# Optimization experiments

Hardware: AMD Instinct MI355X
Metric: run time of the kernel (lower is better)

Reference implementation:

```python
import jax, jax.numpy as jnp
import numpy as np

B, S, D = 2, 2048, 1024
QH, KVH, DH = 16, 4, 64
TOP_K = 128
ROPE_BASE = 10000.0


def _rope(x):
    # x: [B, H, S, DH]; standard LLaMA-style rotate-half RoPE, no freq scaling
    half = DH // 2
    inv_freq = 1.0 / (ROPE_BASE ** (jnp.arange(half, dtype=jnp.float32) / half))
    ang = jnp.arange(S, dtype=jnp.float32)[:, None] * inv_freq[None, :]  # [S, half]
    cos, sin = jnp.cos(ang), jnp.sin(ang)
    x1, x2 = x[..., :half], x[..., half:]
    return jnp.concatenate([x1 * cos - x2 * sin, x2 * cos + x1 * sin], axis=-1)


def setup_inputs() -> dict:
    key = jax.random.key(0)
    ks = jax.random.split(key, 5)
    return {
        "x": jax.random.normal(ks[0], (B, S, D), dtype=jnp.float32),
        "Wq": jax.random.normal(ks[1], (QH * DH, D), dtype=jnp.float32) * 0.02,
        "Wk": jax.random.normal(ks[2], (KVH * DH, D), dtype=jnp.float32) * 0.02,
        "Wv": jax.random.normal(ks[3], (KVH * DH, D), dtype=jnp.float32) * 0.02,
        "Wo": jax.random.normal(ks[4], (D, QH * DH), dtype=jnp.float32) * 0.02,
    }


def reference(x, Wq, Wk, Wv, Wo):
    # projections (Linear, no bias): y = x @ W.T
    q = (x @ Wq.T).reshape(B, S, QH, DH).transpose(0, 2, 1, 3)   # [B,QH,S,DH]
    k = (x @ Wk.T).reshape(B, S, KVH, DH).transpose(0, 2, 1, 3)  # [B,KVH,S,DH]
    v = (x @ Wv.T).reshape(B, S, KVH, DH).transpose(0, 2, 1, 3)
    q = _rope(q)
    k = _rope(k)
    # repeat_kv: GQA expand kv heads to q heads
    rep = QH // KVH
    k = jnp.repeat(k, rep, axis=1)
    v = jnp.repeat(v, rep, axis=1)
    scores = jnp.einsum("bhqd,bhkd->bhqk", q, k) / np.sqrt(DH)  # [B,QH,S,S]
    causal = jnp.triu(jnp.ones((S, S), dtype=bool), k=1)
    scores = jnp.where(causal, -jnp.inf, scores)
    # top-k masking before softmax: keep entries >= per-row k-th largest score
    top_vals = jax.lax.top_k(scores, TOP_K)[0]        # [B,QH,S,TOP_K]
    thr = top_vals[..., -1:]
    scores = jnp.where(scores < thr, -jnp.inf, scores)
    w = jax.nn.softmax(scores, axis=-1)
    out = jnp.einsum("bhqk,bhkd->bhqd", w, v)         # [B,QH,S,DH]
    out = out.transpose(0, 2, 1, 3).reshape(B, S, QH * DH)
    return out @ Wo.T
```

## Files before the change

### kernel.cpp

```cpp
#include <hip/hip_runtime.h>
#include <hip/hip_bf16.h>
#include <hip/hip_fp16.h>
#include <math.h>

constexpr int cB   = 2;
constexpr int cS   = 2048;
constexpr int cD   = 1024;
constexpr int cQH  = 16;
constexpr int cKVH = 4;
constexpr int cDH  = 64;
constexpr int cTOPK = 128;
constexpr int cM   = cB * cS;
constexpr int cNB  = cS / 64;
constexpr int cLSZ = 384;

constexpr int cTI  = 8;
constexpr int cSTR = 130;

constexpr int cNQ  = cQH * cDH;
constexpr int cNK  = cKVH * cDH;
constexpr int cNQKV = cNQ + 2 * cNK;

typedef __attribute__((ext_vector_type(8))) short short8;
typedef __attribute__((ext_vector_type(4))) float floatx4;
typedef _Float16 half8 __attribute__((ext_vector_type(8)));

__device__ inline ushort f2bf(float f) {
    unsigned u = __float_as_uint(f);
    return (ushort)((u + 0x7FFFu + ((u >> 16) & 1u)) >> 16);
}

constexpr int cE0 = cM * cD;
constexpr int cE1 = cE0 + cNQ * cD;
constexpr int cE2 = cE1 + cNK * cD;
constexpr int cE3 = cE2 + cNK * cD;
constexpr int cE4 = cE3 + cD * cQH * cDH;

__global__ void cast_all_bf16(const float* __restrict__ x,
                              const float* __restrict__ wq,
                              const float* __restrict__ wk,
                              const float* __restrict__ wv,
                              const float* __restrict__ wo,
                              ushort* __restrict__ dst) {
    const int i4 = (blockIdx.x * blockDim.x + threadIdx.x) * 4;
    if (i4 >= cE4) return;
    const float* s;
    int off;
    if (i4 < cE0)      { s = x;  off = i4; }
    else if (i4 < cE1) { s = wq; off = i4 - cE0; }
    else if (i4 < cE2) { s = wk; off = i4 - cE1; }
    else if (i4 < cE3) { s = wv; off = i4 - cE2; }
    else               { s = wo; off = i4 - cE3; }
    const float4 v = *(const float4*)(s + off);
    ushort4 r;
    r.x = f2bf(v.x); r.y = f2bf(v.y); r.z = f2bf(v.z); r.w = f2bf(v.w);
    *(ushort4*)(dst + i4) = r;
}

__global__ __launch_bounds__(256) void gemm_bf16_bt(
        const ushort* __restrict__ A, const ushort* __restrict__ W,
        float* __restrict__ C, int M, int N, int K) {
    __shared__ short As[4][128][8];
    __shared__ short Bs[4][128][8];

    const int tid  = threadIdx.x;
    const int lane = tid & 63;
    const int w    = tid >> 6;
    const int wm   = (w & 1) * 64;
    const int wn   = (w >> 1) * 64;
    const int m0   = blockIdx.y * 128;
    const int n0   = blockIdx.x * 128;

    const int quad = lane >> 4;
    const int l16  = lane & 15;

    floatx4 acc[4][4];
    #pragma unroll
    for (int mi = 0; mi < 4; ++mi)
        #pragma unroll
        for (int ni = 0; ni < 4; ++ni)
            acc[mi][ni] = (floatx4){0.f, 0.f, 0.f, 0.f};

    const int sr = tid >> 1;
    const int sh = (tid & 1) * 2;

    for (int k0 = 0; k0 < K; k0 += 32) {
        const ushort* sa = A + (size_t)(m0 + sr) * K + k0 + sh * 8;
        const short8 a0 = *(const short8*)sa;
        const short8 a1 = *(const short8*)(sa + 8);
        const ushort* sw = W + (size_t)(n0 + sr) * K + k0 + sh * 8;
        const short8 b0 = *(const short8*)sw;
        const short8 b1 = *(const short8*)(sw + 8);
        *(short8*)&As[sh][sr][0]     = a0;
        *(short8*)&As[sh + 1][sr][0] = a1;
        *(short8*)&Bs[sh][sr][0]     = b0;
        *(short8*)&Bs[sh + 1][sr][0] = b1;
        __syncthreads();

        short8 af[4], bf[4];
        #pragma unroll
        for (int mi = 0; mi < 4; ++mi)
            af[mi] = *(const short8*)&As[quad][wm + mi * 16 + l16][0];
        #pragma unroll
        for (int ni = 0; ni < 4; ++ni)
            bf[ni] = *(const short8*)&Bs[quad][wn + ni * 16 + l16][0];
        #pragma unroll
        for (int mi = 0; mi < 4; ++mi)
            #pragma unroll
            for (int ni = 0; ni < 4; ++ni)
                acc[mi][ni] = __builtin_amdgcn_mfma_f32_16x16x32_bf16(
                    af[mi], bf[ni], acc[mi][ni], 0, 0, 0);
        __syncthreads();
    }

    #pragma unroll
    for (int mi = 0; mi < 4; ++mi)
        #pragma unroll
        for (int ni = 0; ni < 4; ++ni)
            #pragma unroll
            for (int r = 0; r < 4; ++r) {
                const int row = m0 + wm + mi * 16 + quad * 4 + r;
                const int col = n0 + wn + ni * 16 + l16;
                C[(size_t)row * N + col] = acc[mi][ni][r];
            }
}

__global__ void rope_cast_f16(const float* __restrict__ src,
                              ushort* __restrict__ dst, int H, int total,
                              float scale, int srcStride) {
    int idx = blockIdx.x * blockDim.x + threadIdx.x;
    if (idx >= total) return;
    const int d   = idx & 31;
    const int h   = (idx >> 5) % H;
    const int row = idx / (32 * H);
    const int s   = row % cS;
    const float inv_freq = powf(10000.0f, -(float)d / 32.0f);
    const float ang = (float)s * inv_freq;
    const float c  = cosf(ang);
    const float si = sinf(ang);
    const float* p = src + (size_t)row * srcStride + (size_t)h * cDH;
    const float x1 = p[d];
    const float x2 = p[d + 32];
    const float r1 = (x1 * c - x2 * si) * scale;
    const float r2 = (x2 * c + x1 * si) * scale;
    ushort* o = dst + (size_t)row * H * cDH + (size_t)h * cDH;
    o[d]      = __builtin_bit_cast(ushort, (_Float16)r1);
    o[d + 32] = __builtin_bit_cast(ushort, (_Float16)r2);
}

__global__ void cast_f32_f16_strided(const float* __restrict__ src,
                                     ushort* __restrict__ dst,
                                     int total, int cols, int srcStride) {
    const int i4 = (blockIdx.x * blockDim.x + threadIdx.x) * 4;
    if (i4 >= total) return;
    const int row = i4 / cols;
    const int col = i4 - row * cols;
    const float4 v = *(const float4*)(src + (size_t)row * srcStride + col);
    ushort4 r;
    r.x = __builtin_bit_cast(ushort, (_Float16)v.x);
    r.y = __builtin_bit_cast(ushort, (_Float16)v.y);
    r.z = __builtin_bit_cast(ushort, (_Float16)v.z);
    r.w = __builtin_bit_cast(ushort, (_Float16)v.w);
    *(ushort4*)(dst + i4) = r;
}

__device__ inline unsigned fmap(float f) {
    unsigned u = __float_as_uint(f);
    return (u & 0x80000000u) ? ~u : (u | 0x80000000u);
}
__device__ inline float funmap(unsigned u) {
    unsigned v = (u & 0x80000000u) ? (u & 0x7FFFFFFFu) : ~u;
    return __uint_as_float(v);
}

__global__ __launch_bounds__(512) void attn_tile_kernel(
        const ushort* __restrict__ qf, const ushort* __restrict__ kf,
        const ushort* __restrict__ vf, ushort* __restrict__ out) {
    extern __shared__ char smem[];
    unsigned* stg = (unsigned*)smem;
    unsigned* klA = (unsigned*)smem;
    int*      jlA = (int*)(klA + cTI * cLSZ);

    const int lane = threadIdx.x & 63;
    const int wv   = __builtin_amdgcn_readfirstlane(threadIdx.x >> 6);

    const int x  = blockIdx.x;
    const int it = (cS / cTI - 1) - (x >> 5);
    const int bh = x & 31;
    const int h  = bh & 15;
    const int b  = bh >> 4;
    const int kvh = h >> 2;
    const int i0  = it * cTI;

    const size_t bS = (size_t)b * cS;
    const int l16   = lane & 15;
    const int quad  = lane >> 4;
    const int jperm = ((lane & 3) << 4) + (lane >> 2);
    const int i     = i0 + wv;

    const ushort* qp = qf + ((bS + i0 + (l16 & 7)) * cQH + h) * cDH + quad * 8;
    const half8 a0h = __builtin_bit_cast(half8, *(const uint4*)qp);
    const half8 a1h = __builtin_bit_cast(half8, *(const uint4*)(qp + 32));

    unsigned key[cNB];
    #pragma unroll
    for (int jb = 0; jb < cNB; ++jb) key[jb] = 0u;

    const int nk16   = ((i0 + cTI - 1) >> 4) + 1;
    const int nchunk = (nk16 + 7) >> 3;

    #pragma unroll
    for (int c = 0; c < 16; ++c) {
        if (c >= nchunk) break;
        const int  kb16  = (c << 3) + wv;
        if (kb16 < nk16) {
            const ushort* kp = kf + ((bS + (kb16 << 4) + l16) * cKVH + kvh) * cDH + quad * 8;
            const uint4 b0 = *(const uint4*)kp;
            const uint4 b1 = *(const uint4*)(kp + 32);
            floatx4 acc = (floatx4){0.f, 0.f, 0.f, 0.f};
            acc = __builtin_amdgcn_mfma_f32_16x16x32_f16(
                a0h, __builtin_bit_cast(half8, b0), acc, 0, 0, 0);
            acc = __builtin_amdgcn_mfma_f32_16x16x32_f16(
                a1h, __builtin_bit_cast(half8, b1), acc, 0, 0, 0);
            if (quad < 2) {
                const int jg = (kb16 << 4) + l16;
                unsigned* sp = stg + (c & 1) * (cTI * cSTR) + (wv << 4) + l16;
                #pragma unroll
                for (int r2 = 0; r2 < 4; ++r2) {
                    const int qrow = quad * 4 + r2;
                    sp[qrow * cSTR] = (jg <= i0 + qrow) ? fmap(acc[r2]) : 0u;
                }
            }
        }
        __syncthreads();
        {
            const unsigned* rp = stg + (c & 1) * (cTI * cSTR) + wv * cSTR;
            #pragma unroll
            for (int jj = 0; jj < 2; ++jj) {
                const int j = (c << 7) + (jj << 6) + jperm;
                const unsigned kr = rp[(jj << 6) + jperm];
                key[(c << 1) + jj] = (j <= i) ? kr : 0u;
            }
        }
    }
    __syncthreads();

    const int nb = (i >> 6) + 1;
    unsigned* kl = klA + wv * cLSZ;
    int*      jl = jlA + wv * cLSZ;
    const int vbase0 = (int)(((unsigned)bS * cKVH + kvh) * cDH);

    unsigned um = 0u, un = 0xFFFFFFFFu;
    #pragma unroll
    for (int jb = 0; jb < cNB; ++jb) {
        if (jb >= nb) break;
        const unsigned kk = key[jb];
        um = max(um, kk);
        un = min(un, kk ? kk : 0xFFFFFFFFu);
    }
    #pragma unroll
    for (int off = 32; off >= 1; off >>= 1) {
        um = max(um, (unsigned)__shfl_xor((int)um, off));
        un = min(un, (unsigned)__shfl_xor((int)un, off));
    }
    const float mrow = funmap(um);

    unsigned ustar;
    if (i < cTOPK) {
        ustar = un;
    } else {
        unsigned lo = un, hi = um;
        while (lo < hi) {
            const unsigned d   = hi - lo;
            const unsigned mid = lo + (d >> 1) + (d & 1u);
            int cnt2 = 0;
            #pragma unroll
            for (int jb = 0; jb < cNB; ++jb) {
                if (jb >= nb) break;
                cnt2 += __popcll(__ballot(key[jb] >= mid));
            }
            if (cnt2 == cTOPK) {
                unsigned mn = 0xFFFFFFFFu;
                #pragma unroll
                for (int jb = 0; jb < cNB; ++jb) {
                    if (jb >= nb) break;
                    const unsigned kk = key[jb];
                    mn = min(mn, (kk >= mid) ? kk : 0xFFFFFFFFu);
                }
                #pragma unroll
                for (int off = 32; off >= 1; off >>= 1)
                    mn = min(mn, (unsigned)__shfl_xor((int)mn, off));
                lo = mn;
                break;
            }
            if (cnt2 > cTOPK) lo = mid; else hi = mid - 1u;
        }
        ustar = lo;
    }

    const unsigned long long mlt = (1ull << lane) - 1ull;
    int base = 0;
    #pragma unroll
    for (int jb = 0; jb < cNB; ++jb) {
        if (jb >= nb) break;
        const int j = (jb << 6) + jperm;
        const bool keep = (j <= i) && (key[jb] >= ustar);
        const unsigned long long mk = __ballot(keep);
        const int pos = base + __popcll(mk & mlt);
        if (keep && pos < cLSZ) {
            kl[pos] = key[jb];
            jl[pos] = vbase0 + j * (cKVH * cDH);
        }
        base += __popcll(mk);
    }
    const int cnt = min(base, cLSZ);

    float zp = 0.f;
    for (int t = lane; t < cnt; t += 64) {
        const float s  = funmap(kl[t]);
        const float wt = __expf(s - mrow);
        ((float*)kl)[t] = wt;
        zp += wt;
    }
    #pragma unroll
    for (int off = 32; off >= 1; off >>= 1) zp += __shfl_xor(zp, off);
    const float invZ = 1.0f / zp;

    float ac0 = 0.f, ac1 = 0.f, ac2 = 0.f, ac3 = 0.f;
    float ac4 = 0.f, ac5 = 0.f, ac6 = 0.f, ac7 = 0.f;
    int t = 0;
    #pragma unroll 2
    for (; t + 7 < cnt; t += 8) {
        const float wt0 = ((float*)kl)[t];
        const float wt1 = ((float*)kl)[t + 1];
        const float wt2 = ((float*)kl)[t + 2];
        const float wt3 = ((float*)kl)[t + 3];
        const float wt4 = ((float*)kl)[t + 4];
        const float wt5 = ((float*)kl)[t + 5];
        const float wt6 = ((float*)kl)[t + 6];
        const float wt7 = ((float*)kl)[t + 7];
        const int vo0 = jl[t];
        const int vo1 = jl[t + 1];
        const int vo2 = jl[t + 2];
        const int vo3 = jl[t + 3];
        const int vo4 = jl[t + 4];
        const int vo5 = jl[t + 5];
        const int vo6 = jl[t + 6];
        const int vo7 = jl[t + 7];
        ac0 += wt0 * (float)__builtin_bit_cast(_Float16, vf[vo0 + lane]);
        ac1 += wt1 * (float)__builtin_bit_cast(_Float16, vf[vo1 + lane]);
        ac2 += wt2 * (float)__builtin_bit_cast(_Float16, vf[vo2 + lane]);
        ac3 += wt3 * (float)__builtin_bit_cast(_Float16, vf[vo3 + lane]);
        ac4 += wt4 * (float)__builtin_bit_cast(_Float16, vf[vo4 + lane]);
        ac5 += wt5 * (float)__builtin_bit_cast(_Float16, vf[vo5 + lane]);
        ac6 += wt6 * (float)__builtin_bit_cast(_Float16, vf[vo6 + lane]);
        ac7 += wt7 * (float)__builtin_bit_cast(_Float16, vf[vo7 + lane]);
    }
    for (; t < cnt; ++t) {
        const float wt = ((float*)kl)[t];
        const int   vo = jl[t];
        ac0 += wt * (float)__builtin_bit_cast(_Float16, vf[vo + lane]);
    }
    const float acc = ((ac0 + ac1) + (ac2 + ac3)) + ((ac4 + ac5) + (ac6 + ac7));
    out[((bS + i) * cQH + h) * cDH + lane] = f2bf(acc * invZ);
}

extern "C" void kernel_launch(void* const* d_in, const int* in_sizes, int n_in,
                              void* d_out, int out_size, void* d_ws, size_t ws_size,
                              hipStream_t stream) {
    const float* x  = (const float*)d_in[0];
    const float* Wq = (const float*)d_in[1];
    const float* Wk = (const float*)d_in[2];
    const float* Wv = (const float*)d_in[3];
    const float* Wo = (const float*)d_in[4];
    float* out = (float*)d_out;

    float*  qkvb = (float*)d_ws;
    ushort* xh   = (ushort*)(qkvb + (size_t)cM * cNQKV);
    ushort* Wqh  = xh  + (size_t)cM * cD;
    ushort* Wkh  = Wqh + (size_t)cNQ * cD;
    ushort* Wvh  = Wkh + (size_t)cNK * cD;
    ushort* Woh  = Wvh + (size_t)cNK * cD;
    ushort* abh  = Woh + (size_t)cD * cQH * cDH;
    ushort* qff  = abh + (size_t)cM * cQH * cDH;
    ushort* kff  = qff + (size_t)cM * cQH * cDH;
    ushort* vff  = kff + (size_t)cM * cKVH * cDH;

    dim3 blk(256);

    cast_all_bf16<<<(cE4 / 4 + 255) / 256, blk, 0, stream>>>(
        x, Wq, Wk, Wv, Wo, xh);

    gemm_bf16_bt<<<dim3(cNQKV / 128, cM / 128), blk, 0, stream>>>(
        xh, Wqh, qkvb, cM, cNQKV, cD);

    {
        const int totq = cM * cQH * 32;
        const int totk = cM * cKVH * 32;
        rope_cast_f16<<<(totq + 255) / 256, blk, 0, stream>>>(
            qkvb, qff, cQH, totq, 0.125f, cNQKV);
        rope_cast_f16<<<(totk + 255) / 256, blk, 0, stream>>>(
            qkvb + cNQ, kff, cKVH, totk, 1.0f, cNQKV);
        const int nv = cM * cNK;
        cast_f32_f16_strided<<<(nv / 4 + 255) / 256, blk, 0, stream>>>(
            qkvb + cNQ + cNK, vff, nv, cNK, cNQKV);
    }

    constexpr size_t aSMEM = (size_t)cTI * cLSZ * 8;
    static_assert(2 * cTI * cSTR * 4 <= (int)aSMEM, "staging must fit");
    attn_tile_kernel<<<dim3(32 * (cS / cTI)), dim3(512), aSMEM, stream>>>(
        qff, kff, vff, abh);

    gemm_bf16_bt<<<dim3(cD / 128, cM / 128), blk, 0, stream>>>(abh, Woh, out, cM, cD, cD);
}
```

Measured before the change: 531.8 us.

## Compute top-k P·V with dense MFMA over scattered probabilities and transposed V

The QKV GEMM epilogue now writes V directly as a transposed fp16 buffer, which removes the separate V cast kernel. In the attention kernel, each warp scatters its kept softmax weights into a dense fp16 row of length S in shared memory. All 8 warps then split the key range and run 16x16x32 f16 MFMAs against transposed V, and the partial results are reduced through shared memory. This replaces sparse gathered scalar FMAs with dense tensor-core work, but it processes the whole causal prefix and so does more total FLOPs. It also adds a zero-fill pass over the shared-memory rows and extra synchronisation.

```diff
diff --git a/kernel.cpp b/kernel.cpp
--- a/kernel.cpp
+++ b/kernel.cpp
@@ -16,10 +16,18 @@
 
 constexpr int cTI  = 8;
 constexpr int cSTR = 130;
+constexpr int cPST = 2056;
 
 constexpr int cNQ  = cQH * cDH;
 constexpr int cNK  = cKVH * cDH;
 constexpr int cNQKV = cNQ + 2 * cNK;
+constexpr int cVC0 = cNQ + cNK;
+
+constexpr int cPBY = cTI * cPST * 2;
+constexpr int cKLB = cPBY;
+constexpr int cJSB = cKLB + cTI * cLSZ * 4;
+constexpr int cZB  = cJSB + cTI * cLSZ * 2;
+constexpr int cSMEMA = cZB + 32;
 
 typedef __attribute__((ext_vector_type(8))) short short8;
 typedef __attribute__((ext_vector_type(4))) float floatx4;
@@ -123,6 +131,88 @@
                 const int col = n0 + wn + ni * 16 + l16;
                 C[(size_t)row * N + col] = acc[mi][ni][r];
             }
+}
+
+__global__ __launch_bounds__(256) void gemm_qkv_bf16(
+        const ushort* __restrict__ A, const ushort* __restrict__ W,
+        float* __restrict__ C, ushort* __restrict__ vt, int M, int N, int K) {
+    __shared__ short As[4][128][8];
+    __shared__ short Bs[4][128][8];
+
+    const int tid  = threadIdx.x;
+    const int lane = tid & 63;
+    const int w    = tid >> 6;
+    const int wm   = (w & 1) * 64;
+    const int wn   = (w >> 1) * 64;
+    const int m0   = blockIdx.y * 128;
+    const int n0   = blockIdx.x * 128;
+
+    const int quad = lane >> 4;
+    const int l16  = lane & 15;
+
+    floatx4 acc[4][4];
+    #pragma unroll
+    for (int mi = 0; mi < 4; ++mi)
+        #pragma unroll
+        for (int ni = 0; ni < 4; ++ni)
+            acc[mi][ni] = (floatx4){0.f, 0.f, 0.f, 0.f};
+
+    const int sr = tid >> 1;
+    const int sh = (tid & 1) * 2;
+
+    for (int k0 = 0; k0 < K; k0 += 32) {
+        const ushort* sa = A + (size_t)(m0 + sr) * K + k0 + sh * 8;
+        const short8 a0 = *(const short8*)sa;
+        const short8 a1 = *(const short8*)(sa + 8);
+        const ushort* sw = W + (size_t)(n0 + sr) * K + k0 + sh * 8;
+        const short8 b0 = *(const short8*)sw;
+        const short8 b1 = *(const short8*)(sw + 8);
+        *(short8*)&As[sh][sr][0]     = a0;
+        *(short8*)&As[sh + 1][sr][0] = a1;
+        *(short8*)&Bs[sh][sr][0]     = b0;
+        *(short8*)&Bs[sh + 1][sr][0] = b1;
+        __syncthreads();
+
+        short8 af[4], bf[4];
+        #pragma unroll
+        for (int mi = 0; mi < 4; ++mi)
+            af[mi] = *(const short8*)&As[quad][wm + mi * 16 + l16][0];
+        #pragma unroll
+        for (int ni = 0; ni < 4; ++ni)
+            bf[ni] = *(const short8*)&Bs[quad][wn + ni * 16 + l16][0];
+        #pragma unroll
+        for (int mi = 0; mi < 4; ++mi)
+            #pragma unroll
+            for (int ni = 0; ni < 4; ++ni)
+                acc[mi][ni] = __builtin_amdgcn_mfma_f32_16x16x32_bf16(
+                    af[mi], bf[ni], acc[mi][ni], 0, 0, 0);
+        __syncthreads();
+    }
+
+    #pragma unroll
+    for (int mi = 0; mi < 4; ++mi)
+        #pragma unroll
+        for (int ni = 0; ni < 4; ++ni) {
+            const int col  = n0 + wn + ni * 16 + l16;
+            const int rowb = m0 + wm + mi * 16 + quad * 4;
+            if (col < cVC0) {
+                #pragma unroll
+                for (int r = 0; r < 4; ++r)
+                    C[(size_t)(rowb + r) * N + col] = acc[mi][ni][r];
+            } else {
+                const int vcol = col - cVC0;
+                const int kvh  = vcol >> 6;
+                const int d    = vcol & 63;
+                const int bb   = rowb >> 11;
+                const int jj   = rowb & (cS - 1);
+                ushort4 pk;
+                pk.x = __builtin_bit_cast(ushort, (_Float16)acc[mi][ni][0]);
+                pk.y = __builtin_bit_cast(ushort, (_Float16)acc[mi][ni][1]);
+                pk.z = __builtin_bit_cast(ushort, (_Float16)acc[mi][ni][2]);
+                pk.w = __builtin_bit_cast(ushort, (_Float16)acc[mi][ni][3]);
+                *(ushort4*)(vt + (((size_t)(bb * cKVH + kvh) * cDH + d) << 11) + jj) = pk;
+            }
+        }
 }
 
 __global__ void rope_cast_f16(const float* __restrict__ src,
@@ -148,22 +238,6 @@
     o[d + 32] = __builtin_bit_cast(ushort, (_Float16)r2);
 }
 
-__global__ void cast_f32_f16_strided(const float* __restrict__ src,
-                                     ushort* __restrict__ dst,
-                                     int total, int cols, int srcStride) {
-    const int i4 = (blockIdx.x * blockDim.x + threadIdx.x) * 4;
-    if (i4 >= total) return;
-    const int row = i4 / cols;
-    const int col = i4 - row * cols;
-    const float4 v = *(const float4*)(src + (size_t)row * srcStride + col);
-    ushort4 r;
-    r.x = __builtin_bit_cast(ushort, (_Float16)v.x);
-    r.y = __builtin_bit_cast(ushort, (_Float16)v.y);
-    r.z = __builtin_bit_cast(ushort, (_Float16)v.z);
-    r.w = __builtin_bit_cast(ushort, (_Float16)v.w);
-    *(ushort4*)(dst + i4) = r;
-}
-
 __device__ inline unsigned fmap(float f) {
     unsigned u = __float_as_uint(f);
     return (u & 0x80000000u) ? ~u : (u | 0x80000000u);
@@ -175,11 +249,14 @@
 
 __global__ __launch_bounds__(512) void attn_tile_kernel(
         const ushort* __restrict__ qf, const ushort* __restrict__ kf,
-        const ushort* __restrict__ vf, ushort* __restrict__ out) {
+        const ushort* __restrict__ vt, ushort* __restrict__ out) {
     extern __shared__ char smem[];
+    ushort*   P   = (ushort*)smem;
     unsigned* stg = (unsigned*)smem;
-    unsigned* klA = (unsigned*)smem;
-    int*      jlA = (int*)(klA + cTI * cLSZ);
+    unsigned* klA = (unsigned*)(smem + cKLB);
+    ushort*   jsA = (ushort*)(smem + cJSB);
+    float*    par = (float*)(smem + cKLB);
+    float*    Zs  = (float*)(smem + cZB);
 
     const int lane = threadIdx.x & 63;
     const int wv   = __builtin_amdgcn_readfirstlane(threadIdx.x >> 6);
@@ -245,10 +322,17 @@
     }
     __syncthreads();
 
+    {
+        uint4 z4 = (uint4){0u, 0u, 0u, 0u};
+        uint4* P4 = (uint4*)smem;
+        #pragma unroll 2
+        for (int u = threadIdx.x; u < cPBY / 16; u += 512) P4[u] = z4;
+    }
+    __syncthreads();
+
     const int nb = (i >> 6) + 1;
     unsigned* kl = klA + wv * cLSZ;
-    int*      jl = jlA + wv * cLSZ;
-    const int vbase0 = (int)(((unsigned)bS * cKVH + kvh) * cDH);
+    ushort*   js = jsA + wv * cLSZ;
 
     unsigned um = 0u, un = 0xFFFFFFFFu;
     #pragma unroll
@@ -309,60 +393,60 @@
         const int pos = base + __popcll(mk & mlt);
         if (keep && pos < cLSZ) {
             kl[pos] = key[jb];
-            jl[pos] = vbase0 + j * (cKVH * cDH);
+            js[pos] = (ushort)j;
         }
         base += __popcll(mk);
     }
     const int cnt = min(base, cLSZ);
 
     float zp = 0.f;
+    ushort* Pw = P + wv * cPST;
     for (int t = lane; t < cnt; t += 64) {
         const float s  = funmap(kl[t]);
         const float wt = __expf(s - mrow);
-        ((float*)kl)[t] = wt;
         zp += wt;
+        Pw[js[t]] = __builtin_bit_cast(ushort, (_Float16)wt);
     }
     #pragma unroll
     for (int off = 32; off >= 1; off >>= 1) zp += __shfl_xor(zp, off);
-    const float invZ = 1.0f / zp;
-
-    float ac0 = 0.f, ac1 = 0.f, ac2 = 0.f, ac3 = 0.f;
-    float ac4 = 0.f, ac5 = 0.f, ac6 = 0.f, ac7 = 0.f;
-    int t = 0;
-    #pragma unroll 2
-    for (; t + 7 < cnt; t += 8) {
-        const float wt0 = ((float*)kl)[t];
-        const float wt1 = ((float*)kl)[t + 1];
-        const float wt2 = ((float*)kl)[t + 2];
-        const float wt3 = ((float*)kl)[t + 3];
-        const float wt4 = ((float*)kl)[t + 4];
-        const float wt5 = ((float*)kl)[t + 5];
-        const float wt6 = ((float*)kl)[t + 6];
-        const float wt7 = ((float*)kl)[t + 7];
-        const int vo0 = jl[t];
-        const int vo1 = jl[t + 1];
-        const int vo2 = jl[t + 2];
-        const int vo3 = jl[t + 3];
-        const int vo4 = jl[t + 4];
-        const int vo5 = jl[t + 5];
-        const int vo6 = jl[t + 6];
-        const int vo7 = jl[t + 7];
-        ac0 += wt0 * (float)__builtin_bit_cast(_Float16, vf[vo0 + lane]);
-        ac1 += wt1 * (float)__builtin_bit_cast(_Float16, vf[vo1 + lane]);
-        ac2 += wt2 * (float)__builtin_bit_cast(_Float16, vf[vo2 + lane]);
-        ac3 += wt3 * (float)__builtin_bit_cast(_Float16, vf[vo3 + lane]);
-        ac4 += wt4 * (float)__builtin_bit_cast(_Float16, vf[vo4 + lane]);
-        ac5 += wt5 * (float)__builtin_bit_cast(_Float16, vf[vo5 + lane]);
-        ac6 += wt6 * (float)__builtin_bit_cast(_Float16, vf[vo6 + lane]);
-        ac7 += wt7 * (float)__builtin_bit_cast(_Float16, vf[vo7 + lane]);
-    }
-    for (; t < cnt; ++t) {
-        const float wt = ((float*)kl)[t];
-        const int   vo = jl[t];
-        ac0 += wt * (float)__builtin_bit_cast(_Float16, vf[vo + lane]);
-    }
-    const float acc = ((ac0 + ac1) + (ac2 + ac3)) + ((ac4 + ac5) + (ac6 + ac7));
-    out[((bS + i) * cQH + h) * cDH + lane] = f2bf(acc * invZ);
+    if (lane == 0) Zs[wv] = zp;
+    __syncthreads();
+
+    const int nsl = ((i0 + cTI - 1) >> 5) + 1;
+    floatx4 pacc[4];
+    #pragma unroll
+    for (int db = 0; db < 4; ++db) pacc[db] = (floatx4){0.f, 0.f, 0.f, 0.f};
+
+    const ushort* vtb = vt + (((size_t)(b * cKVH + kvh)) << 17);
+    const int prow = (l16 & 7) * cPST;
+    for (int s = wv; s < nsl; s += 8) {
+        const half8 ap = __builtin_bit_cast(half8,
+            *(const uint4*)(P + prow + s * 32 + quad * 8));
+        #pragma unroll
+        for (int db = 0; db < 4; ++db) {
+            const half8 bp = __builtin_bit_cast(half8,
+                *(const uint4*)(vtb + (((size_t)(db * 16 + l16)) << 11) + s * 32 + quad * 8));
+            pacc[db] = __builtin_amdgcn_mfma_f32_16x16x32_f16(
+                ap, bp, pacc[db], 0, 0, 0);
+        }
+    }
+
+    if (quad < 2) {
+        #pragma unroll
+        for (int db = 0; db < 4; ++db)
+            #pragma unroll
+            for (int r = 0; r < 4; ++r)
+                par[wv * 512 + (quad * 4 + r) * 64 + db * 16 + l16] = pacc[db][r];
+    }
+    __syncthreads();
+
+    {
+        float a = 0.f;
+        #pragma unroll
+        for (int w8 = 0; w8 < 8; ++w8) a += par[w8 * 512 + wv * 64 + lane];
+        const float invZ = 1.0f / Zs[wv];
+        out[((bS + i) * cQH + h) * cDH + lane] = f2bf(a * invZ);
+    }
 }
 
 extern "C" void kernel_launch(void* const* d_in, const int* in_sizes, int n_in,
@@ -384,15 +468,15 @@
     ushort* abh  = Woh + (size_t)cD * cQH * cDH;
     ushort* qff  = abh + (size_t)cM * cQH * cDH;
     ushort* kff  = qff + (size_t)cM * cQH * cDH;
-    ushort* vff  = kff + (size_t)cM * cKVH * cDH;
+    ushort* vt   = kff + (size_t)cM * cKVH * cDH;
 
     dim3 blk(256);
 
     cast_all_bf16<<<(cE4 / 4 + 255) / 256, blk, 0, stream>>>(
         x, Wq, Wk, Wv, Wo, xh);
 
-    gemm_bf16_bt<<<dim3(cNQKV / 128, cM / 128), blk, 0, stream>>>(
-        xh, Wqh, qkvb, cM, cNQKV, cD);
+    gemm_qkv_bf16<<<dim3(cNQKV / 128, cM / 128), blk, 0, stream>>>(
+        xh, Wqh, qkvb, vt, cM, cNQKV, cD);
 
     {
         const int totq = cM * cQH * 32;
@@ -401,15 +485,12 @@
             qkvb, qff, cQH, totq, 0.125f, cNQKV);
         rope_cast_f16<<<(totk + 255) / 256, blk, 0, stream>>>(
             qkvb + cNQ, kff, cKVH, totk, 1.0f, cNQKV);
-        const int nv = cM * cNK;
-        cast_f32_f16_strided<<<(nv / 4 + 255) / 256, blk, 0, stream>>>(
-            qkvb + cNQ + cNK, vff, nv, cNK, cNQKV);
-    }
-
-    constexpr size_t aSMEM = (size_t)cTI * cLSZ * 8;
-    static_assert(2 * cTI * cSTR * 4 <= (int)aSMEM, "staging must fit");
-    attn_tile_kernel<<<dim3(32 * (cS / cTI)), dim3(512), aSMEM, stream>>>(
-        qff, kff, vff, abh);
+    }
+
+    static_assert(2 * cTI * cSTR * 4 <= cPBY, "staging must fit in P region");
+    static_assert(cKLB + 8 * 512 * 4 <= cZB, "partials must fit in kl/jsl");
+    attn_tile_kernel<<<dim3(32 * (cS / cTI)), dim3(512), cSMEMA, stream>>>(
+        qff, kff, vt, abh);
 
     gemm_bf16_bt<<<dim3(cD / 128, cM / 128), blk, 0, stream>>>(abh, Woh, out, cM, cD, cD);
 }
```

New measurement: 541.1 us. Within noise of the previous version (+1.8%).

## Use direct global-to-LDS loads with swizzle in GEMM; prefetch K in scoring

Applied to the files above, without the earlier changes.

The bf16 GEMM now loads tiles straight into LDS with global_load_lds using an XOR-swizzled layout, and reads MFMA fragments through matching swizzled offsets. This skips the register round trip and is meant to reduce LDS bank conflicts. The top-k scoring loop software-prefetches the next K block into registers. It also moves the fmap key transform and causal masking from the staging write to the staging read. The swizzle index math is intricate and a wrong mapping would silently corrupt results.

```diff
diff --git a/kernel.cpp b/kernel.cpp
--- a/kernel.cpp
+++ b/kernel.cpp
@@ -28,6 +28,12 @@
 __device__ inline ushort f2bf(float f) {
     unsigned u = __float_as_uint(f);
     return (ushort)((u + 0x7FFFu + ((u >> 16) & 1u)) >> 16);
+}
+
+__device__ __forceinline__ void glds16(const ushort* g, ushort* l) {
+    __builtin_amdgcn_global_load_lds(
+        (const __attribute__((address_space(1))) unsigned int*)g,
+        (__attribute__((address_space(3))) unsigned int*)l, 16, 0, 0);
 }
 
 constexpr int cE0 = cM * cD;
@@ -60,8 +66,8 @@
 __global__ __launch_bounds__(256) void gemm_bf16_bt(
         const ushort* __restrict__ A, const ushort* __restrict__ W,
         float* __restrict__ C, int M, int N, int K) {
-    __shared__ short As[4][128][8];
-    __shared__ short Bs[4][128][8];
+    __shared__ ushort AsL[128 * 32];
+    __shared__ ushort BsL[128 * 32];
 
     const int tid  = threadIdx.x;
     const int lane = tid & 63;
@@ -70,9 +76,45 @@
     const int wn   = (w >> 1) * 64;
     const int m0   = blockIdx.y * 128;
     const int n0   = blockIdx.x * 128;
-
     const int quad = lane >> 4;
     const int l16  = lane & 15;
+
+    int r0, q0, r1, q1;
+    {
+        const int g5 = (w * 128 + lane) & 31;
+        const int b4 = (g5 >> 4) & 1, b3 = (g5 >> 3) & 1, b2 = (g5 >> 2) & 1;
+        const int b1 = (g5 >> 1) & 1, b0 = g5 & 1;
+        r0 = ((w * 128 + lane) >> 5) * 8 + ((b4 << 2) | (b3 << 1) | (b2 ^ b4));
+        q0 = ((b1 ^ b3) << 1) | (b0 ^ b2 ^ b4);
+    }
+    {
+        const int gI = w * 128 + 64 + lane;
+        const int g5 = gI & 31;
+        const int b4 = (g5 >> 4) & 1, b3 = (g5 >> 3) & 1, b2 = (g5 >> 2) & 1;
+        const int b1 = (g5 >> 1) & 1, b0 = g5 & 1;
+        r1 = (gI >> 5) * 8 + ((b4 << 2) | (b3 << 1) | (b2 ^ b4));
+        q1 = ((b1 ^ b3) << 1) | (b0 ^ b2 ^ b4);
+    }
+    const size_t aOff0 = (size_t)(m0 + r0) * K + q0 * 8;
+    const size_t aOff1 = (size_t)(m0 + r1) * K + q1 * 8;
+    const size_t bOff0 = (size_t)(n0 + r0) * K + q0 * 8;
+    const size_t bOff1 = (size_t)(n0 + r1) * K + q1 * 8;
+    ushort* ldsA0 = AsL + w * 1024;
+    ushort* ldsA1 = AsL + w * 1024 + 512;
+    ushort* ldsB0 = BsL + w * 1024;
+    ushort* ldsB1 = BsL + w * 1024 + 512;
+
+    int eA[4], eB[4];
+    #pragma unroll
+    for (int mi = 0; mi < 4; ++mi) {
+        const int rr = wm + mi * 16 + l16;
+        eA[mi] = (((rr >> 3) * 32) + ((4 * (rr & 7) + quad) ^ (rr & 7))) * 8;
+    }
+    #pragma unroll
+    for (int ni = 0; ni < 4; ++ni) {
+        const int rn = wn + ni * 16 + l16;
+        eB[ni] = (((rn >> 3) * 32) + ((4 * (rn & 7) + quad) ^ (rn & 7))) * 8;
+    }
 
     floatx4 acc[4][4];
     #pragma unroll
@@ -81,29 +123,20 @@
         for (int ni = 0; ni < 4; ++ni)
             acc[mi][ni] = (floatx4){0.f, 0.f, 0.f, 0.f};
 
-    const int sr = tid >> 1;
-    const int sh = (tid & 1) * 2;
-
     for (int k0 = 0; k0 < K; k0 += 32) {
-        const ushort* sa = A + (size_t)(m0 + sr) * K + k0 + sh * 8;
-        const short8 a0 = *(const short8*)sa;
-        const short8 a1 = *(const short8*)(sa + 8);
-        const ushort* sw = W + (size_t)(n0 + sr) * K + k0 + sh * 8;
-        const short8 b0 = *(const short8*)sw;
-        const short8 b1 = *(const short8*)(sw + 8);
-        *(short8*)&As[sh][sr][0]     = a0;
-        *(short8*)&As[sh + 1][sr][0] = a1;
-        *(short8*)&Bs[sh][sr][0]     = b0;
-        *(short8*)&Bs[sh + 1][sr][0] = b1;
+        glds16(A + aOff0 + k0, ldsA0);
+        glds16(A + aOff1 + k0, ldsA1);
+        glds16(W + bOff0 + k0, ldsB0);
+        glds16(W + bOff1 + k0, ldsB1);
         __syncthreads();
 
         short8 af[4], bf[4];
         #pragma unroll
         for (int mi = 0; mi < 4; ++mi)
-            af[mi] = *(const short8*)&As[quad][wm + mi * 16 + l16][0];
+            af[mi] = *(const short8*)(AsL + eA[mi]);
         #pragma unroll
         for (int ni = 0; ni < 4; ++ni)
-            bf[ni] = *(const short8*)&Bs[quad][wn + ni * 16 + l16][0];
+            bf[ni] = *(const short8*)(BsL + eB[ni]);
         #pragma unroll
         for (int mi = 0; mi < 4; ++mi)
             #pragma unroll
@@ -209,27 +242,36 @@
     const int nk16   = ((i0 + cTI - 1) >> 4) + 1;
     const int nchunk = (nk16 + 7) >> 3;
 
+    uint4 pb0, pb1;
+    if (wv < nk16) {
+        const ushort* kp = kf + ((bS + (wv << 4) + l16) * cKVH + kvh) * cDH + quad * 8;
+        pb0 = *(const uint4*)kp;
+        pb1 = *(const uint4*)(kp + 32);
+    }
+
     #pragma unroll
     for (int c = 0; c < 16; ++c) {
         if (c >= nchunk) break;
         const int  kb16  = (c << 3) + wv;
-        if (kb16 < nk16) {
-            const ushort* kp = kf + ((bS + (kb16 << 4) + l16) * cKVH + kvh) * cDH + quad * 8;
-            const uint4 b0 = *(const uint4*)kp;
-            const uint4 b1 = *(const uint4*)(kp + 32);
+        const bool valid = (kb16 < nk16);
+        const uint4 b0 = pb0, b1 = pb1;
+        const int  kb16n = ((c + 1) << 3) + wv;
+        if (kb16n < nk16) {
+            const ushort* kp = kf + ((bS + (kb16n << 4) + l16) * cKVH + kvh) * cDH + quad * 8;
+            pb0 = *(const uint4*)kp;
+            pb1 = *(const uint4*)(kp + 32);
+        }
+        if (valid) {
             floatx4 acc = (floatx4){0.f, 0.f, 0.f, 0.f};
             acc = __builtin_amdgcn_mfma_f32_16x16x32_f16(
                 a0h, __builtin_bit_cast(half8, b0), acc, 0, 0, 0);
             acc = __builtin_amdgcn_mfma_f32_16x16x32_f16(
                 a1h, __builtin_bit_cast(half8, b1), acc, 0, 0, 0);
             if (quad < 2) {
-                const int jg = (kb16 << 4) + l16;
                 unsigned* sp = stg + (c & 1) * (cTI * cSTR) + (wv << 4) + l16;
                 #pragma unroll
-                for (int r2 = 0; r2 < 4; ++r2) {
-                    const int qrow = quad * 4 + r2;
-                    sp[qrow * cSTR] = (jg <= i0 + qrow) ? fmap(acc[r2]) : 0u;
-                }
+                for (int r2 = 0; r2 < 4; ++r2)
+                    sp[(quad * 4 + r2) * cSTR] = __float_as_uint(acc[r2]);
             }
         }
         __syncthreads();
@@ -239,7 +281,8 @@
             for (int jj = 0; jj < 2; ++jj) {
                 const int j = (c << 7) + (jj << 6) + jperm;
                 const unsigned kr = rp[(jj << 6) + jperm];
-                key[(c << 1) + jj] = (j <= i) ? kr : 0u;
+                key[(c << 1) + jj] =
+                    (j <= i) ? fmap(__uint_as_float(kr)) : 0u;
             }
         }
     }
```

Result: no change. 534.9 us (+0.6%).
